# Kernel tuning notes

Hardware: AMD Instinct MI355X
Metric: run time of the kernel (lower is better)

Reference implementation:

```python
import jax, jax.numpy as jnp
import numpy as np

EPS = 1e-5


def _conv1x1(x, w, b=None):
    # x: [B,C,H,W], w: [O,C]
    y = jnp.einsum('bchw,oc->bohw', x, w)
    if b is not None:
        y = y + b[None, :, None, None]
    return y


def _bn(x, g, b, m, v):
    inv = g / jnp.sqrt(v + EPS)
    return x * inv[None, :, None, None] + (b - m * inv)[None, :, None, None]


def setup_inputs() -> dict:
    key = jax.random.key(0)
    ks = jax.random.split(key, 24)
    B, Cin, H, W = 4, 512, 64, 64
    Ci = Cin // 8  # 64
    s = 0.05
    d = {}
    d['x'] = jax.random.normal(ks[0], (B, Cin, H, W), jnp.float32)
    # conv_p1 (BasicConv2d: conv no-bias + BN)
    d['wp1'] = jax.random.normal(ks[1], (Ci, Cin), jnp.float32) * s
    d['gp1'] = jnp.ones((Ci,), jnp.float32)
    d['bp1'] = jnp.zeros((Ci,), jnp.float32)
    d['mp1'] = jax.random.normal(ks[2], (Ci,), jnp.float32) * 0.1
    d['vp1'] = jax.random.uniform(ks[3], (Ci,), jnp.float32, 0.5, 1.5)
    # conv_c1
    d['wc1'] = jax.random.normal(ks[4], (Ci, Cin), jnp.float32) * s
    d['gc1'] = jnp.ones((Ci,), jnp.float32)
    d['bc1'] = jnp.zeros((Ci,), jnp.float32)
    d['mc1'] = jax.random.normal(ks[5], (Ci,), jnp.float32) * 0.1
    d['vc1'] = jax.random.uniform(ks[6], (Ci,), jnp.float32, 0.5, 1.5)
    # PAM 1x1 convs (with bias)
    d['wb'] = jax.random.normal(ks[7], (Ci, Ci), jnp.float32) * s
    d['bb'] = jnp.zeros((Ci,), jnp.float32)
    d['wc2'] = jax.random.normal(ks[8], (Ci, Ci), jnp.float32) * s
    d['bc2'] = jnp.zeros((Ci,), jnp.float32)
    d['wd'] = jax.random.normal(ks[9], (Ci, Ci), jnp.float32) * s
    d['bd'] = jnp.zeros((Ci,), jnp.float32)
    d['alpha'] = jnp.array([0.5], jnp.float32)  # nonzero so attention path is exercised
    d['beta'] = jnp.array([0.5], jnp.float32)
    # out conv
    d['wo'] = jax.random.normal(ks[10], (Cin, Ci), jnp.float32) * s
    d['go'] = jnp.ones((Cin,), jnp.float32)
    d['bo'] = jnp.zeros((Cin,), jnp.float32)
    d['mo'] = jax.random.normal(ks[11], (Cin,), jnp.float32) * 0.1
    d['vo'] = jax.random.uniform(ks[12], (Cin,), jnp.float32, 0.5, 1.5)
    return d


def reference(x, wp1, gp1, bp1, mp1, vp1, wc1, gc1, bc1, mc1, vc1,
              wb, bb, wc2, bc2, wd, bd, alpha, beta, wo, go, bo, mo, vo):
    B, Cin, H, W = x.shape
    HW = H * W

    # --- position branch ---
    fp = _bn(_conv1x1(x, wp1), gp1, bp1, mp1, vp1)          # [B,Ci,H,W]
    Ci = fp.shape[1]
    fb = _conv1x1(fp, wb, bb).reshape(B, Ci, HW)             # query  [B,Ci,HW]
    fc = _conv1x1(fp, wc2, bc2).reshape(B, Ci, HW)           # key    [B,Ci,HW]
    fd = _conv1x1(fp, wd, bd).reshape(B, Ci, HW)             # value  [B,Ci,HW]
    attn_s = jax.nn.softmax(jnp.einsum('bcq,bck->bqk', fb, fc), axis=-1)  # [B,HW,HW]
    feat_ep = jnp.einsum('bck,bqk->bcq', fd, attn_s).reshape(B, Ci, H, W)
    feat_p = alpha[0] * feat_ep + fp

    # --- channel branch ---
    fcb = _bn(_conv1x1(x, wc1), gc1, bc1, mc1, vc1)          # [B,Ci,H,W]
    fa = fcb.reshape(B, Ci, HW)
    attn_c = jnp.einsum('bcn,bdn->bcd', fa, fa)              # [B,Ci,Ci]
    attn_c = jnp.max(attn_c, axis=-1, keepdims=True) - attn_c
    attn_c = jax.nn.softmax(attn_c, axis=-1)
    feat_ec = jnp.einsum('bcd,bdn->bcn', attn_c, fa).reshape(B, Ci, H, W)
    feat_c = beta[0] * feat_ec + fcb

    # --- fuse + out ---
    fusion = feat_p + feat_c
    out = _bn(_conv1x1(fusion, wo), go, bo, mo, vo)          # [B,Cin,H,W]
    return out
```

## Files before the change

kernel.cpp:

```cpp
#include <hip/hip_runtime.h>
#include <hip/hip_bf16.h>

typedef __hip_bfloat16 bf16;
typedef unsigned short u16;
typedef __attribute__((ext_vector_type(8))) short short8;
typedef __attribute__((ext_vector_type(4))) float f32x4;

#define HW 4096
#define NB (64*HW)

__device__ __forceinline__ f32x4 MFMA16(short8 a, short8 b, f32x4 c){
  return __builtin_amdgcn_mfma_f32_16x16x32_bf16(a, b, c, 0, 0, 0);
}

__device__ __forceinline__ short f2bf(float f){
  bf16 h = __float2bfloat16(f);
  return *(short*)&h;
}

__global__ __launch_bounds__(256) void k_const(float* __restrict__ out, float v, int n){
  int i = blockIdx.x*256 + threadIdx.x;
  if (i < n) out[i] = v;
}

__global__ __launch_bounds__(512) void k_prep(
    const float* __restrict__ gp, const float* __restrict__ bp,
    const float* __restrict__ mp, const float* __restrict__ vp,
    const float* __restrict__ gc, const float* __restrict__ bc,
    const float* __restrict__ mc, const float* __restrict__ vc,
    const float* __restrict__ go, const float* __restrict__ bo,
    const float* __restrict__ mo, const float* __restrict__ vo,
    float* __restrict__ bn){
  int t = threadIdx.x;
  if (t < 64){
    float iv = gp[t] * rsqrtf(vp[t] + 1e-5f);
    bn[t] = iv; bn[64+t] = bp[t] - mp[t]*iv;
    float ic = gc[t] * rsqrtf(vc[t] + 1e-5f);
    bn[128+t] = ic; bn[192+t] = bc[t] - mc[t]*ic;
  }
  float io = go[t] * rsqrtf(vo[t] + 1e-5f);
  bn[256+t] = io; bn[768+t] = bo[t] - mo[t]*io;
}

__global__ __launch_bounds__(256) void k_wtrans(
    const float* __restrict__ wp1, const float* __restrict__ wc1,
    const float* __restrict__ wo,
    float* __restrict__ wTin, float* __restrict__ wTout){
  int idx = blockIdx.x*256 + threadIdx.x;
  if (idx < 65536){
    int k = idx >> 7, c = idx & 127;
    wTin[idx] = (c < 64) ? wp1[(size_t)c*512 + k] : wc1[(size_t)(c-64)*512 + k];
  } else {
    int idx2 = idx - 65536;
    int c = idx2 >> 9, o = idx2 & 511;
    wTout[idx2] = wo[(size_t)o*64 + c];
  }
}

__global__ __launch_bounds__(256) void k_conv_in(
    const float* __restrict__ x, const float* __restrict__ wT,
    const float* __restrict__ bn, float* __restrict__ fp, float* __restrict__ fcb){
  const int t = threadIdx.x;
  const int cg = blockIdx.y, b = blockIdx.z;
  const bool isP = cg < 4;
  const int c0 = (cg & 3) * 16;
  const float* inv  = isP ? bn       : bn + 128;
  const float* bias = isP ? bn + 64  : bn + 192;
  float* outp = isP ? fp : fcb;
  const int p = blockIdx.x*256 + t;
  const float* xb = x + (size_t)b*512*HW + p;
  const float* wrow = wT + cg*16;
  float acc[16];
  #pragma unroll
  for (int i = 0; i < 16; i++) acc[i] = 0.f;
  #pragma unroll 8
  for (int k = 0; k < 512; k++){
    float xv = xb[(size_t)k*HW];
    const float4* wr = (const float4*)(wrow + (size_t)k*128);
    float4 w0 = wr[0];
    float4 w1 = wr[1];
    float4 w2 = wr[2];
    float4 w3 = wr[3];
    acc[0]=fmaf(w0.x,xv,acc[0]); acc[1]=fmaf(w0.y,xv,acc[1]); acc[2]=fmaf(w0.z,xv,acc[2]); acc[3]=fmaf(w0.w,xv,acc[3]);
    acc[4]=fmaf(w1.x,xv,acc[4]); acc[5]=fmaf(w1.y,xv,acc[5]); acc[6]=fmaf(w1.z,xv,acc[6]); acc[7]=fmaf(w1.w,xv,acc[7]);
    acc[8]=fmaf(w2.x,xv,acc[8]); acc[9]=fmaf(w2.y,xv,acc[9]); acc[10]=fmaf(w2.z,xv,acc[10]); acc[11]=fmaf(w2.w,xv,acc[11]);
    acc[12]=fmaf(w3.x,xv,acc[12]); acc[13]=fmaf(w3.y,xv,acc[13]); acc[14]=fmaf(w3.z,xv,acc[14]); acc[15]=fmaf(w3.w,xv,acc[15]);
  }
  const size_t base = (size_t)b*NB + p;
  #pragma unroll
  for (int i = 0; i < 16; i++){
    int c = c0 + i;
    outp[base + (size_t)c*HW] = fmaf(acc[i], inv[c], bias[c]);
  }
}

__global__ __launch_bounds__(256) void k_qkv(
    const float* __restrict__ fp,
    const float* __restrict__ wb,  const float* __restrict__ bbv,
    const float* __restrict__ wc2, const float* __restrict__ bc2,
    const float* __restrict__ wd,  const float* __restrict__ bd,
    bf16* __restrict__ fB, bf16* __restrict__ fC, bf16* __restrict__ fD){
  __shared__ __align__(16) float Wl[64][16];
  __shared__ float Bl[16];
  const int t = threadIdx.x;
  const int mg = blockIdx.y, mat = mg >> 2, c0 = (mg & 3)*16, b = blockIdx.z;
  const float* w    = (mat == 0) ? wb  : (mat == 1 ? wc2 : wd);
  const float* bias = (mat == 0) ? bbv : (mat == 1 ? bc2 : bd);
  bf16* outp        = (mat == 0) ? fB  : (mat == 1 ? fC  : fD);
  for (int i = t; i < 1024; i += 256){
    int c = i & 15, k = i >> 4;
    Wl[k][c] = w[(size_t)(c0 + c)*64 + k];
  }
  if (t < 16) Bl[t] = bias[c0 + t];
  __syncthreads();
  const int p = blockIdx.x*512 + t*2;
  const float* in = fp + (size_t)b*NB + p;
  float2 acc[16];
  #pragma unroll
  for (int i = 0; i < 16; i++){ acc[i].x = 0.f; acc[i].y = 0.f; }
  for (int k = 0; k < 64; k++){
    float2 xv = *(const float2*)(in + (size_t)k*HW);
    float4 w0 = *(const float4*)&Wl[k][0];
    float4 w1 = *(const float4*)&Wl[k][4];
    float4 w2 = *(const float4*)&Wl[k][8];
    float4 w3 = *(const float4*)&Wl[k][12];
    float wv[16] = {w0.x,w0.y,w0.z,w0.w, w1.x,w1.y,w1.z,w1.w,
                    w2.x,w2.y,w2.z,w2.w, w3.x,w3.y,w3.z,w3.w};
    #pragma unroll
    for (int i = 0; i < 16; i++){
      acc[i].x = fmaf(wv[i], xv.x, acc[i].x);
      acc[i].y = fmaf(wv[i], xv.y, acc[i].y);
    }
  }
  if (mat < 2){
    bf16* ob = outp + (size_t)b*NB;
    #pragma unroll
    for (int i = 0; i < 16; i += 2){
      __hip_bfloat162 h0 = __float22bfloat162_rn(
          make_float2(acc[i].x + Bl[i], acc[i+1].x + Bl[i+1]));
      __hip_bfloat162 h1 = __float22bfloat162_rn(
          make_float2(acc[i].y + Bl[i], acc[i+1].y + Bl[i+1]));
      *(__hip_bfloat162*)&ob[(size_t)p*64 + c0 + i]     = h0;
      *(__hip_bfloat162*)&ob[(size_t)(p+1)*64 + c0 + i] = h1;
    }
  } else {
    const size_t base = (size_t)b*NB + p;
    #pragma unroll
    for (int i = 0; i < 16; i++){
      float bl = Bl[i];
      __hip_bfloat162 o2 = __float22bfloat162_rn(make_float2(acc[i].x + bl, acc[i].y + bl));
      *(__hip_bfloat162*)&outp[base + (size_t)(c0 + i)*HW] = o2;
    }
  }
}

__global__ __launch_bounds__(256) void k_chan_attn(
    const float* __restrict__ fcb, float* __restrict__ attn){
  __shared__ __align__(16) float rowc[4096];
  __shared__ float red[256];
  __shared__ float Srow[64];
  const int c = blockIdx.x, b = blockIdx.y, t = threadIdx.x;
  const float* fa = fcb + (size_t)b*NB;
  #pragma unroll
  for (int i = 0; i < 4; i++){
    int n = i*1024 + t*4;
    *(float4*)&rowc[n] = *(const float4*)&fa[(size_t)c*HW + n];
  }
  __syncthreads();
  const int d = t >> 2, part = t & 3;
  const float* frow = fa + (size_t)d*HW + part*1024;
  const float* rc = rowc + part*1024;
  float s = 0.f;
  for (int i = 0; i < 1024; i += 4){
    float4 xv = *(const float4*)&frow[i];
    float4 rv = *(const float4*)&rc[i];
    s += xv.x*rv.x + xv.y*rv.y + xv.z*rv.z + xv.w*rv.w;
  }
  red[t] = s;
  __syncthreads();
  if (part == 0) Srow[d] = red[t] + red[t+1] + red[t+2] + red[t+3];
  __syncthreads();
  if (t < 64){
    float z = -Srow[t];
    float m = z;
    #pragma unroll
    for (int off = 32; off; off >>= 1) m = fmaxf(m, __shfl_xor(m, off));
    float e = __expf(fminf(z - m, 0.f));
    float ss = e;
    #pragma unroll
    for (int off = 32; off; off >>= 1) ss += __shfl_xor(ss, off);
    attn[(size_t)b*4096 + (size_t)c*64 + t] = e / ss;
  }
}

__global__ __attribute__((amdgpu_flat_work_group_size(256, 256), amdgpu_waves_per_eu(2, 2)))
void k_pos_attn(
    const u16* __restrict__ fBt, const u16* __restrict__ fCt, const u16* __restrict__ fDv,
    const float* __restrict__ fpl, const float* __restrict__ alphap,
    float* __restrict__ fus){
  __shared__ __align__(16) u16 Kt[2][128*72];
  __shared__ __align__(16) u16 Vt[2][64*136];

  const int t = threadIdx.x;
  const int b = blockIdx.y, q0 = blockIdx.x*32;
  const int wv = t>>6;
  const int g  = wv>>1;
  const int wg = wv&1;
  const int lane = t&63, quad = lane>>4, lr = lane&15;
  const int tg = t & 127;
  const u16* Fb = fBt + (size_t)b*NB;
  const u16* Fc = fCt + (size_t)b*NB;
  const u16* Fd = fDv + (size_t)b*NB;

  const size_t qoff = (size_t)(q0 + wg*16 + lr)*64;
  short8 a0 = *(const short8*)&Fb[qoff + quad*8];
  short8 a1 = *(const short8*)&Fb[qoff + 32 + quad*8];

  const int krbase = ((lr>>2)<<3) + (lr&3);

  float m = -3.0e38f, l = 0.f;
  f32x4 accO[4];
  #pragma unroll
  for (int cs = 0; cs < 4; cs++) accO[cs] = (f32x4){0.f,0.f,0.f,0.f};

  const u16* Ksrc = Fc + (size_t)(g*2048 + tg)*64;
  const u16* Vsrc = Fd + (size_t)(tg>>1)*HW + g*2048 + (tg&1)*64;
  u16* Kdst = &Kt[g][tg*72];
  u16* Vdst = &Vt[g][(tg>>1)*136 + (tg&1)*64];

  for (int tile = 0; tile < 16; ++tile){
    __syncthreads();
    {
      const uint4* ks = (const uint4*)(Ksrc + (size_t)tile*128*64);
      const uint4* vs = (const uint4*)(Vsrc + tile*128);
      #pragma unroll
      for (int i = 0; i < 8; i++) ((uint4*)Kdst)[i] = ks[i];
      #pragma unroll
      for (int i = 0; i < 8; i++) ((uint4*)Vdst)[i] = vs[i];
    }
    __syncthreads();

    f32x4 s[8];
    #pragma unroll
    for (int ks = 0; ks < 8; ks++){
      const int krow = krbase + ((ks>>1)<<5) + ((ks&1)<<2);
      short8 k0 = *(short8*)&Kt[g][krow*72 + quad*8];
      short8 k1 = *(short8*)&Kt[g][krow*72 + 32 + quad*8];
      f32x4 acc = {0.f,0.f,0.f,0.f};
      acc = MFMA16(k0, a0, acc);
      acc = MFMA16(k1, a1, acc);
      s[ks] = acc;
    }

    float t4[8];
    #pragma unroll
    for (int ks = 0; ks < 8; ks++)
      t4[ks] = fmaxf(fmaxf(s[ks][0], s[ks][1]), fmaxf(s[ks][2], s[ks][3]));
    float mx = fmaxf(fmaxf(fmaxf(t4[0],t4[1]), fmaxf(t4[2],t4[3])),
                     fmaxf(fmaxf(t4[4],t4[5]), fmaxf(t4[6],t4[7])));
    mx = fmaxf(mx, __shfl_xor(mx, 16));
    mx = fmaxf(mx, __shfl_xor(mx, 32));
    const float mn = fmaxf(m, mx);
    const float al = __expf(m - mn);
    m = mn;

    short8 pf0, pf1, pf2, pf3;
    float rs = 0.f;
    #pragma unroll
    for (int ks = 0; ks < 8; ks++){
      float e0 = __expf(s[ks][0] - m);
      float e1 = __expf(s[ks][1] - m);
      float e2 = __expf(s[ks][2] - m);
      float e3 = __expf(s[ks][3] - m);
      rs += (e0 + e1) + (e2 + e3);
      const int o = (ks&1)*4;
      short b0 = f2bf(e0), b1 = f2bf(e1), b2 = f2bf(e2), b3 = f2bf(e3);
      if ((ks>>1) == 0){ pf0[o]=b0; pf0[o+1]=b1; pf0[o+2]=b2; pf0[o+3]=b3; }
      else if ((ks>>1) == 1){ pf1[o]=b0; pf1[o+1]=b1; pf1[o+2]=b2; pf1[o+3]=b3; }
      else if ((ks>>1) == 2){ pf2[o]=b0; pf2[o+1]=b1; pf2[o+2]=b2; pf2[o+3]=b3; }
      else            { pf3[o]=b0; pf3[o+1]=b1; pf3[o+2]=b2; pf3[o+3]=b3; }
    }
    rs += __shfl_xor(rs, 16);
    rs += __shfl_xor(rs, 32);
    l = l*al + rs;
    #pragma unroll
    for (int cs = 0; cs < 4; cs++) accO[cs] *= al;

    #pragma unroll
    for (int cs = 0; cs < 4; cs++){
      short8 vf0 = *(short8*)&Vt[g][(cs*16+lr)*136 +  0 + quad*8];
      short8 vf1 = *(short8*)&Vt[g][(cs*16+lr)*136 + 32 + quad*8];
      short8 vf2 = *(short8*)&Vt[g][(cs*16+lr)*136 + 64 + quad*8];
      short8 vf3 = *(short8*)&Vt[g][(cs*16+lr)*136 + 96 + quad*8];
      accO[cs] = MFMA16(vf0, pf0, accO[cs]);
      accO[cs] = MFMA16(vf1, pf1, accO[cs]);
      accO[cs] = MFMA16(vf2, pf2, accO[cs]);
      accO[cs] = MFMA16(vf3, pf3, accO[cs]);
    }
  }

  __syncthreads();
  float* Ol = (float*)&Kt[0][0];
  float* Ml = Ol + 32*69;
  float* Ll = Ml + 32;
  if (g == 1){
    const int row = wg*16 + lr;
    #pragma unroll
    for (int cs = 0; cs < 4; cs++){
      #pragma unroll
      for (int r = 0; r < 4; r++)
        Ol[row*69 + cs*16 + quad*4 + r] = accO[cs][r];
    }
    if (quad == 0){ Ml[row] = m; Ll[row] = l; }
  }
  __syncthreads();
  if (g == 0){
    const float alp = alphap[0];
    const int row = wg*16 + lr;
    const float m1 = Ml[row], l1 = Ll[row];
    const float mt = fmaxf(m, m1);
    const float e0 = __expf(m - mt), e1 = __expf(m1 - mt);
    const float lt = fmaxf(l*e0 + l1*e1, 1e-20f);
    const float sc = alp / lt;
    #pragma unroll
    for (int cs = 0; cs < 4; cs++){
      #pragma unroll
      for (int r = 0; r < 4; r++){
        int idx = row*69 + cs*16 + quad*4 + r;
        Ol[idx] = (accO[cs][r]*e0 + Ol[idx]*e1) * sc;
      }
    }
  }
  __syncthreads();

  {
    const int c = t >> 2, qs = (t & 3) * 8;
    const float* Fp = fpl + (size_t)b*NB + (size_t)c*HW + q0 + qs;
    float* Fo = fus + (size_t)b*NB + (size_t)c*HW + q0 + qs;
    float v[8];
    #pragma unroll
    for (int j = 0; j < 8; j++) v[j] = Ol[(qs+j)*69 + c] + Fp[j];
    *(float4*)&Fo[0] = make_float4(v[0],v[1],v[2],v[3]);
    *(float4*)&Fo[4] = make_float4(v[4],v[5],v[6],v[7]);
  }
}

__global__ __launch_bounds__(256) void k_chan_apply(
    const float* __restrict__ fcb, const float* __restrict__ attn,
    const float* __restrict__ betap, float* __restrict__ fus){
  __shared__ __align__(16) float Ar2[64][8];
  const int t = threadIdx.x;
  const int c0 = blockIdx.y*8, b = blockIdx.z;
  for (int i = t; i < 512; i += 256){
    int d = i >> 3, ci = i & 7;
    Ar2[d][ci] = attn[(size_t)b*4096 + (size_t)(c0 + ci)*64 + d];
  }
  __syncthreads();
  const int p = blockIdx.x*256 + t;
  const float* fa = fcb + (size_t)b*NB;
  float acc[8] = {0.f,0.f,0.f,0.f,0.f,0.f,0.f,0.f};
  for (int d = 0; d < 64; d++){
    float v = fa[(size_t)d*HW + p];
    float4 A0 = *(const float4*)&Ar2[d][0];
    float4 A1 = *(const float4*)&Ar2[d][4];
    acc[0]=fmaf(A0.x,v,acc[0]); acc[1]=fmaf(A0.y,v,acc[1]); acc[2]=fmaf(A0.z,v,acc[2]); acc[3]=fmaf(A0.w,v,acc[3]);
    acc[4]=fmaf(A1.x,v,acc[4]); acc[5]=fmaf(A1.y,v,acc[5]); acc[6]=fmaf(A1.z,v,acc[6]); acc[7]=fmaf(A1.w,v,acc[7]);
  }
  const float be = betap[0];
  #pragma unroll
  for (int i = 0; i < 8; i++){
    size_t idx = (size_t)b*NB + (size_t)(c0 + i)*HW + p;
    fus[idx] += fmaf(be, acc[i], fa[(size_t)(c0 + i)*HW + p]);
  }
}

__global__ __launch_bounds__(256) void k_conv_out(
    const float* __restrict__ fus, const float* __restrict__ woT,
    const float* __restrict__ bn, float* __restrict__ out){
  const int t = threadIdx.x;
  const int o0 = blockIdx.y*16, b = blockIdx.z;
  const int p = blockIdx.x*512 + t*2;
  const float* fu = fus + (size_t)b*NB + p;
  const float* wrow = woT + o0;
  float2 acc[16];
  #pragma unroll
  for (int i = 0; i < 16; i++){ acc[i].x = 0.f; acc[i].y = 0.f; }
  #pragma unroll 4
  for (int c = 0; c < 64; c++){
    float2 xv = *(const float2*)(fu + (size_t)c*HW);
    const float4* wr = (const float4*)(wrow + (size_t)c*512);
    float4 w0 = wr[0];
    float4 w1 = wr[1];
    float4 w2 = wr[2];
    float4 w3 = wr[3];
    float wv[16] = {w0.x,w0.y,w0.z,w0.w, w1.x,w1.y,w1.z,w1.w,
                    w2.x,w2.y,w2.z,w2.w, w3.x,w3.y,w3.z,w3.w};
    #pragma unroll
    for (int i = 0; i < 16; i++){
      acc[i].x = fmaf(wv[i], xv.x, acc[i].x);
      acc[i].y = fmaf(wv[i], xv.y, acc[i].y);
    }
  }
  #pragma unroll
  for (int i = 0; i < 16; i++){
    int o = o0 + i;
    float iv = bn[256+o], bs = bn[768+o];
    float* op = &out[(size_t)b*512*HW + (size_t)o*HW + p];
    op[0] = fmaf(acc[i].x, iv, bs);
    op[1] = fmaf(acc[i].y, iv, bs);
  }
}

extern "C" void kernel_launch(void* const* d_in, const int* in_sizes, int n_in,
                              void* d_out, int out_size, void* d_ws, size_t ws_size,
                              hipStream_t stream){
  static const int dictSz[24] = {8388608,32768,64,64,64,64,32768,64,64,64,64,
                                 4096,64,4096,64,4096,64,1,1,32768,512,512,512,512};
  bool dictOk = (n_in == 24);
  if (dictOk){
    for (int i = 0; i < 24; i++) if (in_sizes[i] != dictSz[i]) dictOk = false;
  }
  bool wsOk = (ws_size >= (size_t)(19u << 20));
  float* out = (float*)d_out;
  if (!dictOk){ k_const<<<(out_size+255)/256, 256, 0, stream>>>(out, 32.f, out_size); return; }
  if (!wsOk)  { k_const<<<(out_size+255)/256, 256, 0, stream>>>(out, 48.f, out_size); return; }

  const float* x    = (const float*)d_in[0];
  const float* wp1  = (const float*)d_in[1];
  const float* gp1  = (const float*)d_in[2];  const float* bp1 = (const float*)d_in[3];
  const float* mp1  = (const float*)d_in[4];  const float* vp1 = (const float*)d_in[5];
  const float* wc1  = (const float*)d_in[6];
  const float* gc1  = (const float*)d_in[7];  const float* bc1 = (const float*)d_in[8];
  const float* mc1  = (const float*)d_in[9];  const float* vc1 = (const float*)d_in[10];
  const float* wb   = (const float*)d_in[11]; const float* bb  = (const float*)d_in[12];
  const float* wc2  = (const float*)d_in[13]; const float* bc2 = (const float*)d_in[14];
  const float* wd   = (const float*)d_in[15]; const float* bd  = (const float*)d_in[16];
  const float* alp  = (const float*)d_in[17]; const float* bet = (const float*)d_in[18];
  const float* wo   = (const float*)d_in[19];
  const float* go   = (const float*)d_in[20]; const float* bo  = (const float*)d_in[21];
  const float* mo   = (const float*)d_in[22]; const float* vo  = (const float*)d_in[23];

  char* w8 = (char*)d_ws;
  float* fp    = (float*)(w8);
  float* fcb   = (float*)(w8 + (4u<<20));
  float* fus   = (float*)(w8 + (8u<<20));
  bf16*  fB    = (bf16*) (w8 + (12u<<20));
  bf16*  fC    = (bf16*) (w8 + (14u<<20));
  bf16*  fD    = (bf16*) (w8 + (16u<<20));
  float* attnc = (float*)(w8 + (18u<<20));
  float* bn    = (float*)(w8 + (18u<<20) + 65536);
  float* wTin  = (float*)(w8 + (18u<<20) + 131072);
  float* wTout = (float*)(w8 + (18u<<20) + 131072 + 262144);

  k_prep<<<1, 512, 0, stream>>>(gp1,bp1,mp1,vp1, gc1,bc1,mc1,vc1, go,bo,mo,vo, bn);
  k_wtrans<<<384, 256, 0, stream>>>(wp1, wc1, wo, wTin, wTout);
  k_conv_in<<<dim3(16,8,4), 256, 0, stream>>>(x, wTin, bn, fp, fcb);
  k_qkv<<<dim3(8,12,4), 256, 0, stream>>>(fp, wb,bb, wc2,bc2, wd,bd, fB, fC, fD);
  k_chan_attn<<<dim3(64,4), 256, 0, stream>>>(fcb, attnc);
  k_pos_attn<<<dim3(128,4), 256, 0, stream>>>((const u16*)fB, (const u16*)fC, (const u16*)fD,
                                              fp, alp, fus);
  k_chan_apply<<<dim3(16,8,4), 256, 0, stream>>>(fcb, attnc, bet, fus);
  k_conv_out<<<dim3(8,32,4), 256, 0, stream>>>(fus, wTout, bn, out);
}
```

Baseline: 314.7 us.

## Load K/V fragments directly from global memory in position attention, drop LDS staging

The position-attention kernel no longer stages K and V tiles in shared memory with two barriers per tile. Each wave now reads its MFMA operand fragments straight from global memory, relying on L1/L2 caching, and shared memory shrinks to the final cross-group merge buffer. This removes the per-tile barriers and LDS round trips and may raise occupancy. In exchange, the two waves of a group now each fetch the same K/V data from global, and the V rows are read with large strides, so memory traffic and latency grow.

```diff
diff --git a/kernel.cpp b/kernel.cpp
--- a/kernel.cpp
+++ b/kernel.cpp
@@ -198,8 +198,7 @@
     const u16* __restrict__ fBt, const u16* __restrict__ fCt, const u16* __restrict__ fDv,
     const float* __restrict__ fpl, const float* __restrict__ alphap,
     float* __restrict__ fus){
-  __shared__ __align__(16) u16 Kt[2][128*72];
-  __shared__ __align__(16) u16 Vt[2][64*136];
+  __shared__ __align__(16) float Ol[32*69 + 64];
 
   const int t = threadIdx.x;
   const int b = blockIdx.y, q0 = blockIdx.x*32;
@@ -207,7 +206,6 @@
   const int g  = wv>>1;
   const int wg = wv&1;
   const int lane = t&63, quad = lane>>4, lr = lane&15;
-  const int tg = t & 127;
   const u16* Fb = fBt + (size_t)b*NB;
   const u16* Fc = fCt + (size_t)b*NB;
   const u16* Fd = fDv + (size_t)b*NB;
@@ -223,29 +221,19 @@
   #pragma unroll
   for (int cs = 0; cs < 4; cs++) accO[cs] = (f32x4){0.f,0.f,0.f,0.f};
 
-  const u16* Ksrc = Fc + (size_t)(g*2048 + tg)*64;
-  const u16* Vsrc = Fd + (size_t)(tg>>1)*HW + g*2048 + (tg&1)*64;
-  u16* Kdst = &Kt[g][tg*72];
-  u16* Vdst = &Vt[g][(tg>>1)*136 + (tg&1)*64];
+  const u16* Kb0 = Fc + (size_t)g*2048*64;
+  const u16* Vb0 = Fd + (size_t)g*2048;
 
   for (int tile = 0; tile < 16; ++tile){
-    __syncthreads();
-    {
-      const uint4* ks = (const uint4*)(Ksrc + (size_t)tile*128*64);
-      const uint4* vs = (const uint4*)(Vsrc + tile*128);
-      #pragma unroll
-      for (int i = 0; i < 8; i++) ((uint4*)Kdst)[i] = ks[i];
-      #pragma unroll
-      for (int i = 0; i < 8; i++) ((uint4*)Vdst)[i] = vs[i];
-    }
-    __syncthreads();
+    const u16* Kb = Kb0 + (size_t)tile*128*64;
+    const u16* Vb = Vb0 + tile*128;
 
     f32x4 s[8];
     #pragma unroll
     for (int ks = 0; ks < 8; ks++){
       const int krow = krbase + ((ks>>1)<<5) + ((ks&1)<<2);
-      short8 k0 = *(short8*)&Kt[g][krow*72 + quad*8];
-      short8 k1 = *(short8*)&Kt[g][krow*72 + 32 + quad*8];
+      short8 k0 = *(const short8*)&Kb[(size_t)krow*64 + quad*8];
+      short8 k1 = *(const short8*)&Kb[(size_t)krow*64 + 32 + quad*8];
       f32x4 acc = {0.f,0.f,0.f,0.f};
       acc = MFMA16(k0, a0, acc);
       acc = MFMA16(k1, a1, acc);
@@ -288,10 +276,11 @@
 
     #pragma unroll
     for (int cs = 0; cs < 4; cs++){
-      short8 vf0 = *(short8*)&Vt[g][(cs*16+lr)*136 +  0 + quad*8];
-      short8 vf1 = *(short8*)&Vt[g][(cs*16+lr)*136 + 32 + quad*8];
-      short8 vf2 = *(short8*)&Vt[g][(cs*16+lr)*136 + 64 + quad*8];
-      short8 vf3 = *(short8*)&Vt[g][(cs*16+lr)*136 + 96 + quad*8];
+      const u16* Vr = Vb + (size_t)(cs*16+lr)*HW;
+      short8 vf0 = *(const short8*)&Vr[ 0 + quad*8];
+      short8 vf1 = *(const short8*)&Vr[32 + quad*8];
+      short8 vf2 = *(const short8*)&Vr[64 + quad*8];
+      short8 vf3 = *(const short8*)&Vr[96 + quad*8];
       accO[cs] = MFMA16(vf0, pf0, accO[cs]);
       accO[cs] = MFMA16(vf1, pf1, accO[cs]);
       accO[cs] = MFMA16(vf2, pf2, accO[cs]);
@@ -299,8 +288,6 @@
     }
   }
 
-  __syncthreads();
-  float* Ol = (float*)&Kt[0][0];
   float* Ml = Ol + 32*69;
   float* Ll = Ml + 32;
   if (g == 1){
```

Measured after the change: 361.5 us. 14.9% more time.
